# Optimization experiments

Measured on AMD Instinct MI355X. Metric: run time of the kernel, lower is better.

## Reference

```python
import jax, jax.numpy as jnp
import numpy as np

B = 32        # number of groups (batch.unique())
L = 512       # max_len (equal-size groups in this setup)
E = 512       # embed_dim
H = 8         # num_heads
N = B * L


def setup_inputs() -> dict:
    key = jax.random.key(0)
    k1, k2, k3 = jax.random.split(key, 3)
    embeddings = jax.random.normal(k1, (N, E), dtype=jnp.float32)
    # sorted group ids; equal group sizes keep max_len static for jit
    batch = jnp.repeat(jnp.arange(B, dtype=jnp.int32), L)
    in_proj_w = jax.random.normal(k2, (3 * E, E), dtype=jnp.float32) * (1.0 / np.sqrt(E))
    in_proj_b = jnp.zeros((3 * E,), dtype=jnp.float32)
    out_proj_w = jax.random.normal(k3, (E, E), dtype=jnp.float32) * (1.0 / np.sqrt(E))
    out_proj_b = jnp.zeros((E,), dtype=jnp.float32)
    return {"embeddings": embeddings, "batch": batch,
            "in_proj_w": in_proj_w, "in_proj_b": in_proj_b,
            "out_proj_w": out_proj_w, "out_proj_b": out_proj_b}


def reference(embeddings, batch, in_proj_w, in_proj_b, out_proj_w, out_proj_b):
    Dh = E // H
    ones = jnp.ones_like(batch, dtype=jnp.int32)
    counts = jax.ops.segment_sum(ones, batch, num_segments=B)          # [B]
    starts = jnp.cumsum(counts) - counts                               # exclusive cumsum
    pos = jnp.arange(N, dtype=jnp.int32) - starts[batch]               # position within group
    # pad ragged -> [B, L, E] (zeros for padding, as in torch code)
    padded = jnp.zeros((B, L, E), dtype=embeddings.dtype).at[batch, pos].set(embeddings)
    # FAITHFUL float attn_mask: +1.0 added to scores outside the valid block
    valid = (jnp.arange(L)[None, :] < counts[:, None]).astype(embeddings.dtype)  # [B, L]
    add_mask = 1.0 - valid[:, :, None] * valid[:, None, :]             # [B, Lq, Lk]

    qkv = padded @ in_proj_w.T + in_proj_b                             # [B, L, 3E]
    q, k, v = jnp.split(qkv, 3, axis=-1)
    q = q.reshape(B, L, H, Dh)
    k = k.reshape(B, L, H, Dh)
    v = v.reshape(B, L, H, Dh)
    scale = 1.0 / np.sqrt(Dh)
    scores = jnp.einsum('bqhd,bkhd->bhqk', q, k) * scale + add_mask[:, None, :, :]
    attn = jax.nn.softmax(scores, axis=-1)
    ctx = jnp.einsum('bhqk,bkhd->bqhd', attn, v).reshape(B, L, E)
    attn_out = ctx @ out_proj_w.T + out_proj_b                         # [B, L, E]
    # max_pool1d over sequence (includes padded query rows, as original)
    return jnp.max(attn_out, axis=1)                                   # [B, E]
```

## Files before the change

kernel.cpp:

```cpp
#include <hip/hip_runtime.h>
#include <math.h>


#define B_ 32
#define L_ 512
#define E_ 512
#define H_ 8
#define DH 64
#define N_ (B_ * L_)
#define EMB_N (N_ * E_)
#define IPW_N (3 * E_ * E_)
#define OPW_N (E_ * E_)

typedef _Float16 f16;
typedef __attribute__((ext_vector_type(8))) _Float16 f16x8;
typedef __attribute__((ext_vector_type(4))) float f32x4;
typedef unsigned short u16;

__device__ __forceinline__ u16 f16_bits(float x) {
    f16 h = (f16)x;
    return *reinterpret_cast<u16*>(&h);
}
__device__ __forceinline__ unsigned pk2(float a, float b) {
    return (unsigned)f16_bits(a) | ((unsigned)f16_bits(b) << 16);
}
__device__ __forceinline__ unsigned pkrtz(float a, float b) {
    auto r = __builtin_amdgcn_cvt_pkrtz(a, b);
    return *reinterpret_cast<unsigned*>(&r);
}
__device__ __forceinline__ void async16(const void* g, void* l) {
    __builtin_amdgcn_global_load_lds(
        (const __attribute__((address_space(1))) void*)g,
        (__attribute__((address_space(3))) void*)l, 16, 0, 0);
}

__device__ __forceinline__ void atomicMaxFloat(float* addr, float val) {
    if (val >= 0.0f) atomicMax((int*)addr, __float_as_int(val));
    else             atomicMin((unsigned int*)addr, __float_as_uint(val));
}

__global__ __launch_bounds__(256) void cvt_kernel(
        const float* __restrict__ emb, const float* __restrict__ ipw,
        const float* __restrict__ opw,
        u16* __restrict__ eh, u16* __restrict__ wh, u16* __restrict__ oh,
        float* __restrict__ out) {
    if (blockIdx.x < 16) {
        int o = blockIdx.x * 1024 + threadIdx.x * 4;
        float4 ninf = make_float4(-INFINITY, -INFINITY, -INFINITY, -INFINITY);
        *(float4*)(out + o) = ninf;
    }
    size_t i = ((size_t)blockIdx.x * 256 + threadIdx.x) * 8;
    const float* src; u16* dst; size_t off;
    if (i < EMB_N)              { src = emb; dst = eh; off = i; }
    else if (i < EMB_N + IPW_N) { src = ipw; dst = wh; off = i - EMB_N; }
    else                        { src = opw; dst = oh; off = i - EMB_N - IPW_N; }
    float4 a = *(const float4*)(src + off);
    float4 b = *(const float4*)(src + off + 4);
    uint4 p;
    p.x = pk2(a.x, a.y); p.y = pk2(a.z, a.w);
    p.z = pk2(b.x, b.y); p.w = pk2(b.z, b.w);
    *(uint4*)(dst + off) = p;
}

__global__ __launch_bounds__(512) void qkv_mfma(
        const u16* __restrict__ Wg, const u16* __restrict__ Eg,
        const float* __restrict__ bias,
        u16* __restrict__ qg, u16* __restrict__ kg, u16* __restrict__ vg) {
    __shared__ u16 Ah[2][128 * 32];
    __shared__ u16 Bh[2][256 * 32];
    const int tok0 = blockIdx.x * 256, row0 = blockIdx.y * 128;
    const int tid = threadIdx.x, wave = tid >> 6, lane = tid & 63;
    const int quad = lane >> 4, c = lane & 15;
    const int ww = wave & 1, wt = wave >> 1;
    const int sw = (quad ^ ((c >> 1) & 3)) * 8;
    const bool vblk = (row0 >= 1024);

    f32x4 zero = {0.f, 0.f, 0.f, 0.f};
    f32x4 acc[4][4];
#pragma unroll
    for (int i = 0; i < 4; i++)
#pragma unroll
        for (int j = 0; j < 4; j++) acc[i][j] = zero;

    auto stage = [&](int buf, int kt) {
        {
            int chunk = wave * 64 + lane;
            int r = chunk >> 2, g = chunk & 3;
            int pos = g ^ ((r >> 1) & 3);
            async16(Wg + (size_t)(row0 + r) * E_ + kt * 32 + pos * 8,
                    &Ah[buf][wave * 512]);
        }
#pragma unroll
        for (int it = 0; it < 2; it++) {
            int chunk = (it * 8 + wave) * 64 + lane;
            int r = chunk >> 2, g = chunk & 3;
            int pos = g ^ ((r >> 1) & 3);
            async16(Eg + (size_t)(tok0 + r) * E_ + kt * 32 + pos * 8,
                    &Bh[buf][(it * 8 + wave) * 512]);
        }
    };

    stage(0, 0);
    for (int kt = 0; kt < 16; kt++) {
        __syncthreads();
        if (kt < 15) stage((kt + 1) & 1, kt + 1);
        const int buf = kt & 1;
        f16x8 mf[4], nf[4];
        if (!vblk) {
#pragma unroll
            for (int i = 0; i < 4; i++)
                mf[i] = *(const f16x8*)&Ah[buf][(ww * 64 + i * 16 + c) * 32 + sw];
#pragma unroll
            for (int j = 0; j < 4; j++)
                nf[j] = *(const f16x8*)&Bh[buf][(wt * 64 + j * 16 + c) * 32 + sw];
        } else {
#pragma unroll
            for (int i = 0; i < 4; i++)
                mf[i] = *(const f16x8*)&Bh[buf][(wt * 64 + i * 16 + c) * 32 + sw];
#pragma unroll
            for (int j = 0; j < 4; j++)
                nf[j] = *(const f16x8*)&Ah[buf][(ww * 64 + j * 16 + c) * 32 + sw];
        }
#pragma unroll
        for (int i = 0; i < 4; i++)
#pragma unroll
            for (int j = 0; j < 4; j++)
                acc[i][j] = __builtin_amdgcn_mfma_f32_16x16x32_f16(mf[i], nf[j], acc[i][j], 0, 0, 0);
    }

    if (!vblk) {
        const int which = row0 >> 9;
        u16* dst = which ? kg : qg;
        const float scale = which ? 1.0f : 0.18033688f;
        const int h = (((row0 & 511) + ww * 64) >> 6);
#pragma unroll
        for (int i = 0; i < 4; i++) {
            const int d0 = i * 16 + quad * 4;
            float4 bv = *(const float4*)(bias + row0 + ww * 64 + d0);
            const int dch = i * 2 + (quad >> 1);
#pragma unroll
            for (int j = 0; j < 4; j++) {
                int n = tok0 + wt * 64 + j * 16 + c;
                int bb = n >> 9, l = n & 511;
                uint2 st;
                st.x = pk2((acc[i][j][0] + bv.x) * scale, (acc[i][j][1] + bv.y) * scale);
                st.y = pk2((acc[i][j][2] + bv.z) * scale, (acc[i][j][3] + bv.w) * scale);
                size_t addr = (size_t)(bb * H_ + h) * 32768 +
                              (l >> 4) * 1024 + dch * 128 + (l & 15) * 8 + (quad & 1) * 4;
                *(uint2*)(dst + addr) = st;
            }
        }
    } else {
        const int bb = tok0 >> 9;
        const int l0 = (tok0 & 511) + wt * 64;
        const int tt = l0 >> 6;
        const int h = (((row0 & 511) + ww * 64) >> 6);
#pragma unroll
        for (int j = 0; j < 4; j++) {
            int mw = row0 + ww * 64 + j * 16 + c;
            int d = mw & 63;
            float bv = bias[mw];
#pragma unroll
            for (int i = 0; i < 4; i++) {
                uint2 st;
                st.x = pk2(acc[i][j][0] + bv, acc[i][j][1] + bv);
                st.y = pk2(acc[i][j][2] + bv, acc[i][j][3] + bv);
                size_t addr = (size_t)(bb * H_ + h) * 32768 + tt * 4096 +
                              j * 1024 + (i * 2 + (quad >> 1)) * 128 +
                              c * 8 + (quad & 1) * 4;
                *(uint2*)(vg + addr) = st;
            }
        }
    }
}

__global__ __launch_bounds__(256, 2) void attn_mfma(
        const u16* __restrict__ qg, const u16* __restrict__ kg,
        const u16* __restrict__ vg, u16* __restrict__ ctx) {
    __shared__ u16 ps[4][2][2][1088];
    const int qt = blockIdx.x, h = blockIdx.y, b = blockIdx.z;
    const int tid = threadIdx.x, wave = tid >> 6, lane = tid & 63;
    const int quad = lane >> 4, c = lane & 15;
    const size_t base = (size_t)(b * H_ + h) * 32768;
    const int lane8 = lane * 8;

    f16x8 qf[2][2];
#pragma unroll
    for (int rs = 0; rs < 2; rs++) {
        const size_t qb = base + (size_t)(qt * 8 + wave * 2 + rs) * 1024;
#pragma unroll
        for (int kk = 0; kk < 2; kk++)
            qf[rs][kk] = *(const f16x8*)(qg + qb + kk * 512 + lane8);
    }

    f32x4 zero = {0.f, 0.f, 0.f, 0.f};
    const f32x4 m6 = {-6.f, -6.f, -6.f, -6.f};
    f16x8 ones;
#pragma unroll
    for (int i = 0; i < 8; i++) ones[i] = (f16)1.0f;

    f32x4 Of[2][4];
    f32x4 lacc[2];
#pragma unroll
    for (int rs = 0; rs < 2; rs++) {
        lacc[rs] = zero;
#pragma unroll
        for (int j = 0; j < 4; j++) Of[rs][j] = zero;
    }

    f16x8 kf[2][4][2], vf[2][2][4];
#pragma unroll
    for (int jj = 0; jj < 4; jj++)
#pragma unroll
        for (int kk = 0; kk < 2; kk++)
            kf[0][jj][kk] = *(const f16x8*)(kg + base + jj * 1024 + kk * 512 + lane8);
#pragma unroll
    for (int kk = 0; kk < 2; kk++)
#pragma unroll
        for (int j = 0; j < 4; j++)
            vf[0][kk][j] = *(const f16x8*)(vg + base + j * 1024 + kk * 512 + lane8);

#pragma unroll
    for (int kt = 0; kt < 8; kt++) {
        const int cur = kt & 1, nx = cur ^ 1;
        if (kt < 7) {
            const size_t tbn = base + (size_t)(kt + 1) * 4096;
#pragma unroll
            for (int jj = 0; jj < 4; jj++)
#pragma unroll
                for (int kk = 0; kk < 2; kk++)
                    kf[nx][jj][kk] = *(const f16x8*)(kg + tbn + jj * 1024 + kk * 512 + lane8);
#pragma unroll
            for (int kk = 0; kk < 2; kk++)
#pragma unroll
                for (int j = 0; j < 4; j++)
                    vf[nx][kk][j] = *(const f16x8*)(vg + tbn + j * 1024 + kk * 512 + lane8);
        }

#pragma unroll
        for (int rs = 0; rs < 2; rs++) {
            f32x4 Sf[4];
            __builtin_amdgcn_s_setprio(1);
#pragma unroll
            for (int jj = 0; jj < 4; jj++) {
                Sf[jj] = m6;
#pragma unroll
                for (int kk = 0; kk < 2; kk++)
                    Sf[jj] = __builtin_amdgcn_mfma_f32_16x16x32_f16(kf[cur][jj][kk], qf[rs][kk], Sf[jj], 0, 0, 0);
            }
            __builtin_amdgcn_s_setprio(0);
            u16* psw = &ps[wave][cur][rs][0];
#pragma unroll
            for (int jj = 0; jj < 4; jj++) {
                float p0 = exp2f(Sf[jj][0]), p1 = exp2f(Sf[jj][1]);
                float p2 = exp2f(Sf[jj][2]), p3 = exp2f(Sf[jj][3]);
                int addr = (2 * jj + (quad >> 1)) * 136 + c * 8 + 4 * (quad & 1);
                *(uint2*)&psw[addr] = make_uint2(pkrtz(p0, p1), pkrtz(p2, p3));
            }
            f16x8 pf0 = *(const f16x8*)&psw[(0 + quad) * 136 + c * 8];
            f16x8 pf1 = *(const f16x8*)&psw[(4 + quad) * 136 + c * 8];
            __builtin_amdgcn_s_setprio(1);
            lacc[rs] = __builtin_amdgcn_mfma_f32_16x16x32_f16(ones, pf0, lacc[rs], 0, 0, 0);
            lacc[rs] = __builtin_amdgcn_mfma_f32_16x16x32_f16(ones, pf1, lacc[rs], 0, 0, 0);
#pragma unroll
            for (int j = 0; j < 4; j++) {
                Of[rs][j] = __builtin_amdgcn_mfma_f32_16x16x32_f16(vf[cur][0][j], pf0, Of[rs][j], 0, 0, 0);
                Of[rs][j] = __builtin_amdgcn_mfma_f32_16x16x32_f16(vf[cur][1][j], pf1, Of[rs][j], 0, 0, 0);
            }
            __builtin_amdgcn_s_setprio(0);
        }
    }

#pragma unroll
    for (int rs = 0; rs < 2; rs++) {
        float inv = 1.0f / lacc[rs][0];
        int n = b * L_ + qt * 128 + wave * 32 + rs * 16 + c;
#pragma unroll
        for (int j = 0; j < 4; j++) {
            int d0 = j * 16 + quad * 4;
            uint2 st;
            st.x = pk2(Of[rs][j][0] * inv, Of[rs][j][1] * inv);
            st.y = pk2(Of[rs][j][2] * inv, Of[rs][j][3] * inv);
            *(uint2*)(ctx + (size_t)n * E_ + h * DH + d0) = st;
        }
    }
}

__global__ __launch_bounds__(256) void proj_mfma(
        const u16* __restrict__ Ag, const u16* __restrict__ Bg,
        const float* __restrict__ bias, float* __restrict__ out) {
    __shared__ u16 Ah[2][128 * 32], Bh[2][128 * 32];
    __shared__ float red[2][128];
    const int row0 = blockIdx.x * 128, col0 = blockIdx.y * 128;
    const int tid = threadIdx.x, wave = tid >> 6, lane = tid & 63;
    const int quad = lane >> 4, c = lane & 15;
    const int wr = (wave >> 1) * 64, wc = (wave & 1) * 64;
    const int sw = (quad ^ ((c >> 1) & 3)) * 8;

    f32x4 zero = {0.f, 0.f, 0.f, 0.f};
    f32x4 acc[4][4];
#pragma unroll
    for (int i = 0; i < 4; i++)
#pragma unroll
        for (int j = 0; j < 4; j++) acc[i][j] = zero;

    auto stage = [&](int buf, int kt) {
#pragma unroll
        for (int it = 0; it < 2; it++) {
            int chunk = (wave * 2 + it) * 64 + lane;
            int r = chunk >> 2, g = chunk & 3;
            int pos = g ^ ((r >> 1) & 3);
            int lbase = (wave * 2 + it) * 512;
            async16(Ag + (size_t)(row0 + r) * E_ + kt * 32 + pos * 8, &Ah[buf][lbase]);
            async16(Bg + (size_t)(col0 + r) * E_ + kt * 32 + pos * 8, &Bh[buf][lbase]);
        }
    };

    stage(0, 0);
    for (int kt = 0; kt < 16; kt++) {
        __syncthreads();
        if (kt < 15) stage((kt + 1) & 1, kt + 1);
        const int buf = kt & 1;
        f16x8 af[4], bf[4];
#pragma unroll
        for (int i = 0; i < 4; i++)
            af[i] = *(const f16x8*)&Ah[buf][(wr + i * 16 + c) * 32 + sw];
#pragma unroll
        for (int j = 0; j < 4; j++)
            bf[j] = *(const f16x8*)&Bh[buf][(wc + j * 16 + c) * 32 + sw];
#pragma unroll
        for (int i = 0; i < 4; i++)
#pragma unroll
            for (int j = 0; j < 4; j++)
                acc[i][j] = __builtin_amdgcn_mfma_f32_16x16x32_f16(af[i], bf[j], acc[i][j], 0, 0, 0);
    }

    float cm[4];
#pragma unroll
    for (int j = 0; j < 4; j++) {
        cm[j] = -INFINITY;
#pragma unroll
        for (int i = 0; i < 4; i++)
#pragma unroll
            for (int r = 0; r < 4; r++) cm[j] = fmaxf(cm[j], acc[i][j][r]);
        cm[j] = fmaxf(cm[j], __shfl_xor(cm[j], 16));
        cm[j] = fmaxf(cm[j], __shfl_xor(cm[j], 32));
    }
    if (quad == 0)
#pragma unroll
        for (int j = 0; j < 4; j++) red[wave >> 1][wc + j * 16 + c] = cm[j];
    __syncthreads();
    if (tid < 128) {
        int bb = row0 >> 9;
        float m = fmaxf(red[0][tid], red[1][tid]) + bias[col0 + tid];
        atomicMaxFloat(&out[(size_t)bb * E_ + col0 + tid], m);
    }
}

extern "C" void kernel_launch(void* const* d_in, const int* in_sizes, int n_in,
                              void* d_out, int out_size, void* d_ws, size_t ws_size,
                              hipStream_t stream) {
    const float* emb = (const float*)d_in[0];
    const float* ipw = (const float*)d_in[2];
    const float* ipb = (const float*)d_in[3];
    const float* opw = (const float*)d_in[4];
    const float* opb = (const float*)d_in[5];
    float* out = (float*)d_out;

    u16* eh  = (u16*)d_ws;
    u16* wh  = eh + EMB_N;
    u16* oh  = wh + IPW_N;
    u16* qg  = oh + OPW_N;
    u16* kg  = qg + (size_t)N_ * E_;
    u16* vg  = kg + (size_t)N_ * E_;
    u16* ctx = vg + (size_t)N_ * E_;

    cvt_kernel<<<(EMB_N + IPW_N + OPW_N) / (256 * 8), 256, 0, stream>>>(
        emb, ipw, opw, eh, wh, oh, out);
    qkv_mfma<<<dim3(N_ / 256, (3 * E_) / 128), 512, 0, stream>>>(
        wh, eh, ipb, qg, kg, vg);
    attn_mfma<<<dim3(L_ / 128, H_, B_), 256, 0, stream>>>(qg, kg, vg, ctx);
    proj_mfma<<<dim3(N_ / 128, E_ / 128), 256, 0, stream>>>(ctx, oh, opb, out);
}
```

Baseline: 161.7 us.

## Keep softmax probabilities in registers and permute the V layout to match

The attention kernel no longer stages exp'd scores through shared memory to rebuild MFMA B-operand fragments. Each lane packs its own S accumulator values directly into the P fragments. To keep the PV product correct, the projection kernel now writes V in a permuted key-order layout that matches this register-resident P ordering, and it uses 16-byte stores instead of 8-byte ones. This removes LDS writes and reads and frees LDS per block. It depends on the key permutation being consistent between the V layout and the P packing.

```diff
diff --git a/kernel.cpp b/kernel.cpp
--- a/kernel.cpp
+++ b/kernel.cpp
@@ -158,17 +158,17 @@
 #pragma unroll
         for (int j = 0; j < 4; j++) {
             int mw = row0 + ww * 64 + j * 16 + c;
-            int d = mw & 63;
             float bv = bias[mw];
 #pragma unroll
-            for (int i = 0; i < 4; i++) {
-                uint2 st;
-                st.x = pk2(acc[i][j][0] + bv, acc[i][j][1] + bv);
-                st.y = pk2(acc[i][j][2] + bv, acc[i][j][3] + bv);
+            for (int ip = 0; ip < 2; ip++) {
+                uint4 st;
+                st.x = pk2(acc[2 * ip][j][0] + bv, acc[2 * ip][j][1] + bv);
+                st.y = pk2(acc[2 * ip][j][2] + bv, acc[2 * ip][j][3] + bv);
+                st.z = pk2(acc[2 * ip + 1][j][0] + bv, acc[2 * ip + 1][j][1] + bv);
+                st.w = pk2(acc[2 * ip + 1][j][2] + bv, acc[2 * ip + 1][j][3] + bv);
                 size_t addr = (size_t)(bb * H_ + h) * 32768 + tt * 4096 +
-                              j * 1024 + (i * 2 + (quad >> 1)) * 128 +
-                              c * 8 + (quad & 1) * 4;
-                *(uint2*)(vg + addr) = st;
+                              j * 1024 + ip * 512 + quad * 128 + c * 8;
+                *(uint4*)(vg + addr) = st;
             }
         }
     }
@@ -177,7 +177,6 @@
 __global__ __launch_bounds__(256, 2) void attn_mfma(
         const u16* __restrict__ qg, const u16* __restrict__ kg,
         const u16* __restrict__ vg, u16* __restrict__ ctx) {
-    __shared__ u16 ps[4][2][2][1088];
     const int qt = blockIdx.x, h = blockIdx.y, b = blockIdx.z;
     const int tid = threadIdx.x, wave = tid >> 6, lane = tid & 63;
     const int quad = lane >> 4, c = lane & 15;
@@ -249,16 +248,16 @@
                     Sf[jj] = __builtin_amdgcn_mfma_f32_16x16x32_f16(kf[cur][jj][kk], qf[rs][kk], Sf[jj], 0, 0, 0);
             }
             __builtin_amdgcn_s_setprio(0);
-            u16* psw = &ps[wave][cur][rs][0];
+            unsigned w[8];
 #pragma unroll
             for (int jj = 0; jj < 4; jj++) {
-                float p0 = exp2f(Sf[jj][0]), p1 = exp2f(Sf[jj][1]);
-                float p2 = exp2f(Sf[jj][2]), p3 = exp2f(Sf[jj][3]);
-                int addr = (2 * jj + (quad >> 1)) * 136 + c * 8 + 4 * (quad & 1);
-                *(uint2*)&psw[addr] = make_uint2(pkrtz(p0, p1), pkrtz(p2, p3));
-            }
-            f16x8 pf0 = *(const f16x8*)&psw[(0 + quad) * 136 + c * 8];
-            f16x8 pf1 = *(const f16x8*)&psw[(4 + quad) * 136 + c * 8];
+                w[2 * jj]     = pkrtz(exp2f(Sf[jj][0]), exp2f(Sf[jj][1]));
+                w[2 * jj + 1] = pkrtz(exp2f(Sf[jj][2]), exp2f(Sf[jj][3]));
+            }
+            union { uint4 u; f16x8 v; } u0, u1;
+            u0.u = make_uint4(w[0], w[1], w[2], w[3]);
+            u1.u = make_uint4(w[4], w[5], w[6], w[7]);
+            f16x8 pf0 = u0.v, pf1 = u1.v;
             __builtin_amdgcn_s_setprio(1);
             lacc[rs] = __builtin_amdgcn_mfma_f32_16x16x32_f16(ones, pf0, lacc[rs], 0, 0, 0);
             lacc[rs] = __builtin_amdgcn_mfma_f32_16x16x32_f16(ones, pf1, lacc[rs], 0, 0, 0);
```

Measured after the change: 165.3 us. +2.3%, slower.
